# Optimization experiments

Hardware: AMD Instinct MI355X
Metric: run time of the kernel (lower is better)

Reference implementation:

```python
import jax, jax.numpy as jnp
import numpy as np


def setup_inputs() -> dict:
    key = jax.random.key(0)
    x = jax.random.normal(key, (64, 512, 40, 40), dtype=jnp.float32)
    return {"x": x}


def reference(x) -> jnp.ndarray:
    # unfold(k=3, pad=1, stride=1) followed by fold back to (40, 40) is an
    # overlap-sum: each output pixel is the sum of its 3x3 neighborhood
    # (zero-padded at borders) == depthwise conv with a 3x3 ones kernel.
    C = x.shape[1]
    kernel = jnp.ones((C, 1, 3, 3), dtype=x.dtype)  # depthwise ones kernel
    return jax.lax.conv_general_dilated(
        x, kernel,
        window_strides=(1, 1),
        padding=((1, 1), (1, 1)),
        dimension_numbers=("NCHW", "OIHW", "NCHW"),
        feature_group_count=C,
    )
```

## Files before the change

### kernel.cpp

```cpp
#include <hip/hip_runtime.h>


#define NV 400
#define ROW4 10

typedef float f32x4 __attribute__((ext_vector_type(4)));

__device__ __forceinline__ float4 hsum4(const float4 c, float lf, float rt) {
    float4 h;
    h.x = lf  + c.x + c.y;
    h.y = c.x + c.y + c.z;
    h.z = c.y + c.z + c.w;
    h.w = c.z + c.w + rt;
    return h;
}

__device__ __forceinline__ void nt_store4(float4* p, const float4 v) {
    f32x4 nv;
    nv.x = v.x; nv.y = v.y; nv.z = v.z; nv.w = v.w;
    __builtin_nontemporal_store(nv, reinterpret_cast<f32x4*>(p));
}

__global__ __launch_bounds__(256) void overlap_sum_3x3(
    const float* __restrict__ in, float* __restrict__ out)
{
    __shared__ float4 s_a[NV];
    __shared__ float4 s_h[NV];

    const int t = threadIdx.x;
    const size_t po = (size_t)blockIdx.x * NV;
    const float4* __restrict__ src = reinterpret_cast<const float4*>(in) + po;
    float4*       __restrict__ dst = reinterpret_cast<float4*>(out) + po;

    const bool two = (t < NV - 256);
    float4 v0 = src[t];
    float4 v1;
    s_a[t] = v0;
    if (two) { v1 = src[t + 256]; s_a[t + 256] = v1; }
    __syncthreads();

    const int x40 = t % ROW4;
    float lf0 = (x40 > 0)        ? s_a[t - 1].w : 0.0f;
    float rt0 = (x40 < ROW4 - 1) ? s_a[t + 1].x : 0.0f;
    float4 h0 = hsum4(v0, lf0, rt0);
    s_h[t] = h0;

    float4 h1;
    if (two) {
        const int j  = t + 256;
        const int x41 = j % ROW4;
        float lf1 = (x41 > 0)        ? s_a[j - 1].w : 0.0f;
        float rt1 = (x41 < ROW4 - 1) ? s_a[j + 1].x : 0.0f;
        h1 = hsum4(v1, lf1, rt1);
        s_h[j] = h1;
    }
    __syncthreads();

    {
        float4 o = h0;
        if (t >= ROW4) {
            const float4 u = s_h[t - ROW4];
            o.x += u.x; o.y += u.y; o.z += u.z; o.w += u.w;
        }
        const float4 d = s_h[t + ROW4];
        o.x += d.x; o.y += d.y; o.z += d.z; o.w += d.w;
        nt_store4(&dst[t], o);
    }
    if (two) {
        const int j = t + 256;
        float4 o = h1;
        const float4 u = s_h[j - ROW4];
        o.x += u.x; o.y += u.y; o.z += u.z; o.w += u.w;
        if (j < NV - ROW4) {
            const float4 d = s_h[j + ROW4];
            o.x += d.x; o.y += d.y; o.z += d.z; o.w += d.w;
        }
        nt_store4(&dst[j], o);
    }
}

extern "C" void kernel_launch(void* const* d_in, const int* in_sizes, int n_in,
                              void* d_out, int out_size, void* d_ws, size_t ws_size,
                              hipStream_t stream) {
    const float* x = (const float*)d_in[0];
    float* out = (float*)d_out;
    const int n_planes = in_sizes[0] / (NV * 4);
    overlap_sum_3x3<<<n_planes, 256, 0, stream>>>(x, out);
}
```

Measured before the change: 63.54 us.

## Make blocks persistent over planes and prefetch the next plane during stores

```diff
diff --git a/kernel.cpp b/kernel.cpp
--- a/kernel.cpp
+++ b/kernel.cpp
@@ -3,6 +3,7 @@
 
 #define NV 400
 #define ROW4 10
+#define NBLOCKS 2048
 
 typedef float f32x4 __attribute__((ext_vector_type(4)));
 
@@ -22,60 +23,84 @@
 }
 
 __global__ __launch_bounds__(256) void overlap_sum_3x3(
-    const float* __restrict__ in, float* __restrict__ out)
+    const float* __restrict__ in, float* __restrict__ out, int n_planes)
 {
     __shared__ float4 s_a[NV];
     __shared__ float4 s_h[NV];
 
-    const int t = threadIdx.x;
-    const size_t po = (size_t)blockIdx.x * NV;
-    const float4* __restrict__ src = reinterpret_cast<const float4*>(in) + po;
-    float4*       __restrict__ dst = reinterpret_cast<float4*>(out) + po;
+    const int t   = threadIdx.x;
+    const bool two = (t < NV - 256);
+    const int x40 = t % ROW4;
+    const int x41 = (t + 256) % ROW4;
 
-    const bool two = (t < NV - 256);
-    float4 v0 = src[t];
-    float4 v1;
-    s_a[t] = v0;
-    if (two) { v1 = src[t + 256]; s_a[t + 256] = v1; }
-    __syncthreads();
+    int p = blockIdx.x;
+    if (p >= n_planes) return;
 
-    const int x40 = t % ROW4;
-    float lf0 = (x40 > 0)        ? s_a[t - 1].w : 0.0f;
-    float rt0 = (x40 < ROW4 - 1) ? s_a[t + 1].x : 0.0f;
-    float4 h0 = hsum4(v0, lf0, rt0);
-    s_h[t] = h0;
+    float4 v0, v1;
+    {
+        const float4* __restrict__ src =
+            reinterpret_cast<const float4*>(in) + (size_t)p * NV;
+        v0 = src[t];
+        if (two) v1 = src[t + 256];
+    }
 
-    float4 h1;
-    if (two) {
-        const int j  = t + 256;
-        const int x41 = j % ROW4;
-        float lf1 = (x41 > 0)        ? s_a[j - 1].w : 0.0f;
-        float rt1 = (x41 < ROW4 - 1) ? s_a[j + 1].x : 0.0f;
-        h1 = hsum4(v1, lf1, rt1);
-        s_h[j] = h1;
-    }
-    __syncthreads();
+    while (true) {
+        s_a[t] = v0;
+        if (two) s_a[t + 256] = v1;
+        __syncthreads();
 
-    {
-        float4 o = h0;
-        if (t >= ROW4) {
-            const float4 u = s_h[t - ROW4];
+        float lf0 = (x40 > 0)        ? s_a[t - 1].w : 0.0f;
+        float rt0 = (x40 < ROW4 - 1) ? s_a[t + 1].x : 0.0f;
+        float4 h0 = hsum4(v0, lf0, rt0);
+        s_h[t] = h0;
+
+        float4 h1;
+        if (two) {
+            float lf1 = (x41 > 0)        ? s_a[t + 255].w : 0.0f;
+            float rt1 = (x41 < ROW4 - 1) ? s_a[t + 257].x : 0.0f;
+            h1 = hsum4(v1, lf1, rt1);
+            s_h[t + 256] = h1;
+        }
+        __syncthreads();
+
+        const int pn = p + NBLOCKS;
+        const bool more = (pn < n_planes);
+        float4 n0, n1;
+        if (more) {
+            const float4* __restrict__ srcn =
+                reinterpret_cast<const float4*>(in) + (size_t)pn * NV;
+            n0 = srcn[t];
+            if (two) n1 = srcn[t + 256];
+        }
+
+        float4* __restrict__ dst =
+            reinterpret_cast<float4*>(out) + (size_t)p * NV;
+        {
+            float4 o = h0;
+            if (t >= ROW4) {
+                const float4 u = s_h[t - ROW4];
+                o.x += u.x; o.y += u.y; o.z += u.z; o.w += u.w;
+            }
+            const float4 d = s_h[t + ROW4];
+            o.x += d.x; o.y += d.y; o.z += d.z; o.w += d.w;
+            nt_store4(&dst[t], o);
+        }
+        if (two) {
+            const int j = t + 256;
+            float4 o = h1;
+            const float4 u = s_h[j - ROW4];
             o.x += u.x; o.y += u.y; o.z += u.z; o.w += u.w;
+            if (j < NV - ROW4) {
+                const float4 d = s_h[j + ROW4];
+                o.x += d.x; o.y += d.y; o.z += d.z; o.w += d.w;
+            }
+            nt_store4(&dst[j], o);
         }
-        const float4 d = s_h[t + ROW4];
-        o.x += d.x; o.y += d.y; o.z += d.z; o.w += d.w;
-        nt_store4(&dst[t], o);
-    }
-    if (two) {
-        const int j = t + 256;
-        float4 o = h1;
-        const float4 u = s_h[j - ROW4];
-        o.x += u.x; o.y += u.y; o.z += u.z; o.w += u.w;
-        if (j < NV - ROW4) {
-            const float4 d = s_h[j + ROW4];
-            o.x += d.x; o.y += d.y; o.z += d.z; o.w += d.w;
-        }
-        nt_store4(&dst[j], o);
+
+        if (!more) break;
+        p = pn;
+        v0 = n0;
+        if (two) v1 = n1;
     }
 }
 
@@ -85,5 +110,6 @@
     const float* x = (const float*)d_in[0];
     float* out = (float*)d_out;
     const int n_planes = in_sizes[0] / (NV * 4);
-    overlap_sum_3x3<<<n_planes, 256, 0, stream>>>(x, out);
+    const int grid = (n_planes < NBLOCKS) ? n_planes : NBLOCKS;
+    overlap_sum_3x3<<<grid, 256, 0, stream>>>(x, out, n_planes);
 }
```

After: 67.05 us. 1.06x slower.
